# Performance work log

Measured on AMD Instinct MI355X. Metric: run time of the kernel, lower is better.

Reference implementation:

```python
import jax, jax.numpy as jnp
import numpy as np

HUGE = jnp.float32(1e31)  # ops.HUGE_INT


def setup_inputs() -> dict:
    key = jax.random.key(0)
    ks = jax.random.split(key, 11)
    B, A = 2048, 256
    NE, NR = 100000, 1000
    DE, DR, DH = 128, 128, 256
    act = DE + DR  # action_dim = W1 hidden width
    return {
        "e": jax.random.randint(ks[0], (B,), 0, NE),
        "q": jax.random.randint(ks[1], (B,), 0, NR),
        "H": jax.random.normal(ks[2], (B, DH), jnp.float32),
        "r_space": jax.random.randint(ks[3], (B, A), 0, NR),
        "r_mask": jnp.ones((B, A), jnp.float32),
        "entity_emb": jax.random.normal(ks[4], (NE, DE), jnp.float32),
        "rel_emb": jax.random.normal(ks[5], (NR, DR), jnp.float32),
        "W1": jax.random.normal(ks[6], (DE + DH + DR, act), jnp.float32) * 0.05,
        "b1": jnp.zeros((act,), jnp.float32),
        "W2": jax.random.normal(ks[7], (act, DR), jnp.float32) * 0.05,
        "b2": jnp.zeros((DR,), jnp.float32),
    }


def reference(e, q, H, r_space, r_mask, entity_emb, rel_emb, W1, b1, W2, b2):
    # Gather node / query embeddings (kg.get_entity_embeddings / get_relation_embeddings)
    E = entity_emb[e]              # [B, DE]
    Q = rel_emb[q]                 # [B, DR]
    X = jnp.concatenate([E, H, Q], axis=-1)        # [B, DE+DH+DR]
    X = jax.nn.relu(X @ W1 + b1)                   # W1 + ReLU
    X = X @ W2 + b2                                # W2 -> [B, DR]
    # Gather candidate relation embeddings for the (padded) action space
    R = rel_emb[r_space]                           # [B, A, DR]
    logit = jnp.einsum("bad,bd->ba", R, X)        # squeeze(R @ X.unsqueeze(2))
    logit = logit - (1.0 - r_mask) * HUGE          # mask invalid actions
    dist = jax.nn.softmax(logit, axis=-1)          # [B, A]
    entropy = -jnp.sum(dist * jnp.log(jnp.clip(dist, 1e-20, None)), axis=-1)  # ops.entropy
    return dist, entropy
```

## Files before the change

### kernel.cpp

```cpp
#include <hip/hip_runtime.h>


#define DE   128
#define DH   256
#define DR   128
#define DIN  512
#define ACT  256
#define AA   256
#define BB   8
#define NR   1000
#define SCL  1008

#define XS_P 520
#define HS_P 264
#define X2_P 136

#define W2B_OFF 16384
#define RB_OFF  20480
#define PREP_T  36608

typedef __attribute__((ext_vector_type(4))) float f32x4;
typedef __attribute__((ext_vector_type(8))) short s16x8;
typedef unsigned int u32;
typedef unsigned short u16;

#define MFMA(a,b,c) __builtin_amdgcn_mfma_f32_16x16x32_bf16(a, b, c, 0, 0, 0)

__device__ __forceinline__ u32 b16(float x) {
    u32 u = __float_as_uint(x);
    return (u + 0x7FFFu + ((u >> 16) & 1u)) >> 16;
}
__device__ __forceinline__ float b16f(u32 h) { return __uint_as_float(h << 16); }
__device__ __forceinline__ u32 pack2(float a, float b) { return b16(a) | (b16(b) << 16); }

__device__ __forceinline__ s16x8 asfrag(uint4 v) {
    union { uint4 u; s16x8 s; } c; c.u = v; return c.s;
}

__global__ __launch_bounds__(256) void prep_kernel(
    const float* __restrict__ W1, const float* __restrict__ W2,
    const float* __restrict__ rel_emb, uint4* __restrict__ wsb)
{
    const int id = blockIdx.x * 256 + threadIdx.x;
    const int l  = id & 63;
    const int tl = id >> 6;
    const int kb_l = (l >> 4) * 8;
    const int n_l  = l & 15;
    float f[8];
    if (tl < 256) {
        const int kt = tl >> 4, nt = tl & 15;
        const int kb = kt * 32 + kb_l, n = nt * 16 + n_l;
        #pragma unroll
        for (int i = 0; i < 8; ++i) f[i] = W1[(size_t)(kb + i) * ACT + n];
    } else if (tl < 320) {
        const int t2 = tl - 256;
        const int kt = t2 >> 3, nt = t2 & 7;
        const int kb = kt * 32 + kb_l, n = nt * 16 + n_l;
        #pragma unroll
        for (int i = 0; i < 8; ++i) f[i] = W2[(size_t)(kb + i) * DR + n];
    } else {
        const int t3 = tl - 320;
        const int nt = t3 >> 2, kt = t3 & 3;
        const int kb = kt * 32 + kb_l, n = nt * 16 + n_l;
        #pragma unroll
        for (int i = 0; i < 8; ++i)
            f[i] = (n < NR) ? rel_emb[(size_t)n * DR + kb + i] : 0.f;
    }
    uint4 o;
    o.x = pack2(f[0], f[1]); o.y = pack2(f[2], f[3]);
    o.z = pack2(f[4], f[5]); o.w = pack2(f[6], f[7]);
    wsb[id] = o;
}

__global__ __launch_bounds__(512, 2) void policy_kernel(
    const int*   __restrict__ e,
    const int*   __restrict__ q,
    const float* __restrict__ H,
    const int*   __restrict__ r_space,
    const float* __restrict__ r_mask,
    const float* __restrict__ entity_emb,
    const float* __restrict__ rel_emb,
    const float* __restrict__ b1,
    const float* __restrict__ b2,
    const uint4* __restrict__ wsb,
    float* __restrict__ dist_out,
    float* __restrict__ ent_out)
{
    const int t  = threadIdx.x;
    const int b0 = blockIdx.x * BB;
    const int l  = t & 63;
    const int w  = t >> 6;
    const int m  = l & 15;
    const int pl = m >> 3;
    const int rw = m & 7;
    const int kb_l = (l >> 4) * 8;

    __shared__ __align__(16) u16 xbf[2][BB][XS_P];
    __shared__ __align__(16) u16 hbf[2][BB][HS_P];
    __shared__ __align__(16) u16 x2bf[2][BB][X2_P];
    __shared__ float scoreL[BB * SCL];

    int   ridx[4];
    float msk [4];
    #pragma unroll
    for (int c = 0; c < 4; ++c) {
        ridx[c] = r_space[(size_t)(b0 + w) * AA + l + 64 * c];
        msk [c] = r_mask [(size_t)(b0 + w) * AA + l + 64 * c];
    }

    #pragma unroll
    for (int u = 0; u < 2; ++u) {
        const int j   = t + u * 512;
        const int row = j & 7;
        const int kq  = (j >> 3) * 4;
        const int sb  = b0 + row;
        float4 v;
        if (kq < DE)            v = *(const float4*)&entity_emb[(size_t)e[sb] * DE + kq];
        else if (kq < DE + DH)  v = *(const float4*)&H[(size_t)sb * DH + (kq - DE)];
        else                    v = *(const float4*)&rel_emb[(size_t)q[sb] * DR + (kq - DE - DH)];
        const float f[4] = {v.x, v.y, v.z, v.w};
        u32 hi[4], lo[4];
        #pragma unroll
        for (int i = 0; i < 4; ++i) {
            hi[i] = b16(f[i]);
            lo[i] = b16(f[i] - b16f(hi[i]));
        }
        uint2 ph, plv;
        ph.x  = hi[0] | (hi[1] << 16); ph.y  = hi[2] | (hi[3] << 16);
        plv.x = lo[0] | (lo[1] << 16); plv.y = lo[2] | (lo[3] << 16);
        *(uint2*)&xbf[0][row][kq] = ph;
        *(uint2*)&xbf[1][row][kq] = plv;
    }
    __syncthreads();

    {
        f32x4 acc0 = {0.f, 0.f, 0.f, 0.f};
        f32x4 acc1 = {0.f, 0.f, 0.f, 0.f};
        const int nt0 = 2 * w, nt1 = 2 * w + 1;
        const u16* abase = &xbf[pl][rw][kb_l];
        #pragma unroll
        for (int kt = 0; kt < 16; ++kt) {
            const uint4 af  = *(const uint4*)(abase + kt * 32);
            const uint4 bv0 = wsb[(size_t)(kt * 16 + nt0) * 64 + l];
            const uint4 bv1 = wsb[(size_t)(kt * 16 + nt1) * 64 + l];
            acc0 = MFMA(asfrag(af), asfrag(bv0), acc0);
            acc1 = MFMA(asfrag(af), asfrag(bv1), acc1);
        }
        #pragma unroll
        for (int v = 0; v < 4; ++v) {
            acc0[v] += __shfl_xor(acc0[v], 32, 64);
            acc1[v] += __shfl_xor(acc1[v], 32, 64);
        }
        if (l < 32) {
            const int r4 = (l >> 4) * 4;
            const int n0 = nt0 * 16 + m, n1 = nt1 * 16 + m;
            const float bb0 = b1[n0], bb1 = b1[n1];
            #pragma unroll
            for (int v = 0; v < 4; ++v) {
                const float h0 = fmaxf(acc0[v] + bb0, 0.f);
                const float h1 = fmaxf(acc1[v] + bb1, 0.f);
                const u32 h0h = b16(h0), h1h = b16(h1);
                hbf[0][r4 + v][n0] = (u16)h0h;
                hbf[1][r4 + v][n0] = (u16)b16(h0 - b16f(h0h));
                hbf[0][r4 + v][n1] = (u16)h1h;
                hbf[1][r4 + v][n1] = (u16)b16(h1 - b16f(h1h));
            }
        }
    }
    __syncthreads();

    {
        f32x4 acc = {0.f, 0.f, 0.f, 0.f};
        const u16* abase = &hbf[pl][rw][kb_l];
        #pragma unroll
        for (int kt = 0; kt < 8; ++kt) {
            const uint4 af = *(const uint4*)(abase + kt * 32);
            const uint4 bv = wsb[(size_t)(W2B_OFF + (kt * 8 + w) * 64 + l)];
            acc = MFMA(asfrag(af), asfrag(bv), acc);
        }
        #pragma unroll
        for (int v = 0; v < 4; ++v) acc[v] += __shfl_xor(acc[v], 32, 64);
        if (l < 32) {
            const int r4 = (l >> 4) * 4;
            const int n  = w * 16 + m;
            const float bb = b2[n];
            #pragma unroll
            for (int v = 0; v < 4; ++v) {
                const float x2 = acc[v] + bb;
                const u32 xh = b16(x2);
                x2bf[0][r4 + v][n] = (u16)xh;
                x2bf[1][r4 + v][n] = (u16)b16(x2 - b16f(xh));
            }
        }
    }
    __syncthreads();

    {
        uint4 sf[4];
        const u16* abase = &x2bf[pl][rw][kb_l];
        #pragma unroll
        for (int kt = 0; kt < 4; ++kt)
            sf[kt] = *(const uint4*)(abase + kt * 32);
        #pragma unroll 2
        for (int i = 0; i < 8; ++i) {
            const int nt = w * 8 + i;
            if (nt >= 63) break;
            f32x4 acc = {0.f, 0.f, 0.f, 0.f};
            #pragma unroll
            for (int kt = 0; kt < 4; ++kt) {
                const uint4 bv = wsb[(size_t)(RB_OFF + (nt * 4 + kt) * 64 + l)];
                acc = MFMA(asfrag(sf[kt]), asfrag(bv), acc);
            }
            #pragma unroll
            for (int v = 0; v < 4; ++v) acc[v] += __shfl_xor(acc[v], 32, 64);
            if (l < 32) {
                const int r4 = (l >> 4) * 4;
                const int n  = nt * 16 + m;
                #pragma unroll
                for (int v = 0; v < 4; ++v)
                    scoreL[(r4 + v) * SCL + n] = acc[v];
            }
        }
    }
    __syncthreads();

    {
        float lg[4];
        #pragma unroll
        for (int c = 0; c < 4; ++c)
            lg[c] = scoreL[w * SCL + ridx[c]] - (1.0f - msk[c]) * 1e31f;

        float mx = fmaxf(fmaxf(lg[0], lg[1]), fmaxf(lg[2], lg[3]));
        #pragma unroll
        for (int off = 32; off >= 1; off >>= 1)
            mx = fmaxf(mx, __shfl_xor(mx, off, 64));

        float p[4], S = 0.f, SLa = 0.f;
        #pragma unroll
        for (int c = 0; c < 4; ++c) {
            const float z = lg[c] - mx;
            p[c] = __expf(z);
            S   += p[c];
            SLa += p[c] * z;
        }
        #pragma unroll
        for (int off = 32; off >= 1; off >>= 1) {
            S   += __shfl_xor(S,   off, 64);
            SLa += __shfl_xor(SLa, off, 64);
        }

        const float inv = 1.0f / S;
        #pragma unroll
        for (int c = 0; c < 4; ++c)
            dist_out[(size_t)(b0 + w) * AA + l + 64 * c] = p[c] * inv;
        if (l == 0)
            ent_out[b0 + w] = __logf(S) - SLa * inv;
    }
}

extern "C" void kernel_launch(void* const* d_in, const int* in_sizes, int n_in,
                              void* d_out, int out_size, void* d_ws, size_t ws_size,
                              hipStream_t stream) {
    const int*   e          = (const int*)  d_in[0];
    const int*   q          = (const int*)  d_in[1];
    const float* H          = (const float*)d_in[2];
    const int*   r_space    = (const int*)  d_in[3];
    const float* r_mask     = (const float*)d_in[4];
    const float* entity_emb = (const float*)d_in[5];
    const float* rel_emb    = (const float*)d_in[6];
    const float* W1         = (const float*)d_in[7];
    const float* b1         = (const float*)d_in[8];
    const float* W2         = (const float*)d_in[9];
    const float* b2         = (const float*)d_in[10];

    const int B = in_sizes[0];
    float* dist_out = (float*)d_out;
    float* ent_out  = (float*)d_out + (size_t)B * AA;
    uint4* wsb      = (uint4*)d_ws;

    prep_kernel<<<PREP_T / 256, 256, 0, stream>>>(W1, W2, rel_emb, wsb);
    policy_kernel<<<B / BB, 512, 0, stream>>>(
        e, q, H, r_space, r_mask, entity_emb, rel_emb,
        b1, b2, wsb, dist_out, ent_out);
}
```

Baseline: 22.68 us.

## Double policy kernel block to 1024 threads, splitting layer-1 and score tiles across 16 waves

Launches the policy kernel with 1024 threads (16 waves) per block instead of 512. Each wave now computes one W1 output tile instead of two, and the relation-score GEMM spreads its 63 tiles over 16 waves, four each. The W2 layer and the softmax/entropy stage stay on the first 8 waves, so half the waves idle there. The aim is more parallelism and shorter per-wave MFMA chains. The cost is higher register pressure under launch_bounds(1024,2) and idle waves in the serial stages.

```diff
diff --git a/kernel.cpp b/kernel.cpp
--- a/kernel.cpp
+++ b/kernel.cpp
@@ -72,7 +72,7 @@
     wsb[id] = o;
 }
 
-__global__ __launch_bounds__(512, 2) void policy_kernel(
+__global__ __launch_bounds__(1024, 2) void policy_kernel(
     const int*   __restrict__ e,
     const int*   __restrict__ q,
     const float* __restrict__ H,
@@ -102,17 +102,17 @@
 
     int   ridx[4];
     float msk [4];
-    #pragma unroll
-    for (int c = 0; c < 4; ++c) {
-        ridx[c] = r_space[(size_t)(b0 + w) * AA + l + 64 * c];
-        msk [c] = r_mask [(size_t)(b0 + w) * AA + l + 64 * c];
-    }
-
-    #pragma unroll
-    for (int u = 0; u < 2; ++u) {
-        const int j   = t + u * 512;
-        const int row = j & 7;
-        const int kq  = (j >> 3) * 4;
+    if (w < 8) {
+        #pragma unroll
+        for (int c = 0; c < 4; ++c) {
+            ridx[c] = r_space[(size_t)(b0 + w) * AA + l + 64 * c];
+            msk [c] = r_mask [(size_t)(b0 + w) * AA + l + 64 * c];
+        }
+    }
+
+    {
+        const int row = t & 7;
+        const int kq  = (t >> 3) * 4;
         const int sb  = b0 + row;
         float4 v;
         if (kq < DE)            v = *(const float4*)&entity_emb[(size_t)e[sb] * DE + kq];
@@ -134,42 +134,33 @@
     __syncthreads();
 
     {
-        f32x4 acc0 = {0.f, 0.f, 0.f, 0.f};
-        f32x4 acc1 = {0.f, 0.f, 0.f, 0.f};
-        const int nt0 = 2 * w, nt1 = 2 * w + 1;
+        f32x4 acc = {0.f, 0.f, 0.f, 0.f};
         const u16* abase = &xbf[pl][rw][kb_l];
         #pragma unroll
         for (int kt = 0; kt < 16; ++kt) {
-            const uint4 af  = *(const uint4*)(abase + kt * 32);
-            const uint4 bv0 = wsb[(size_t)(kt * 16 + nt0) * 64 + l];
-            const uint4 bv1 = wsb[(size_t)(kt * 16 + nt1) * 64 + l];
-            acc0 = MFMA(asfrag(af), asfrag(bv0), acc0);
-            acc1 = MFMA(asfrag(af), asfrag(bv1), acc1);
-        }
-        #pragma unroll
-        for (int v = 0; v < 4; ++v) {
-            acc0[v] += __shfl_xor(acc0[v], 32, 64);
-            acc1[v] += __shfl_xor(acc1[v], 32, 64);
-        }
+            const uint4 af = *(const uint4*)(abase + kt * 32);
+            const uint4 bv = wsb[(size_t)(kt * 16 + w) * 64 + l];
+            acc = MFMA(asfrag(af), asfrag(bv), acc);
+        }
+        #pragma unroll
+        for (int v = 0; v < 4; ++v)
+            acc[v] += __shfl_xor(acc[v], 32, 64);
         if (l < 32) {
             const int r4 = (l >> 4) * 4;
-            const int n0 = nt0 * 16 + m, n1 = nt1 * 16 + m;
-            const float bb0 = b1[n0], bb1 = b1[n1];
+            const int n  = w * 16 + m;
+            const float bb = b1[n];
             #pragma unroll
             for (int v = 0; v < 4; ++v) {
-                const float h0 = fmaxf(acc0[v] + bb0, 0.f);
-                const float h1 = fmaxf(acc1[v] + bb1, 0.f);
-                const u32 h0h = b16(h0), h1h = b16(h1);
-                hbf[0][r4 + v][n0] = (u16)h0h;
-                hbf[1][r4 + v][n0] = (u16)b16(h0 - b16f(h0h));
-                hbf[0][r4 + v][n1] = (u16)h1h;
-                hbf[1][r4 + v][n1] = (u16)b16(h1 - b16f(h1h));
-            }
-        }
-    }
-    __syncthreads();
-
-    {
+                const float h = fmaxf(acc[v] + bb, 0.f);
+                const u32 hh = b16(h);
+                hbf[0][r4 + v][n] = (u16)hh;
+                hbf[1][r4 + v][n] = (u16)b16(h - b16f(hh));
+            }
+        }
+    }
+    __syncthreads();
+
+    if (w < 8) {
         f32x4 acc = {0.f, 0.f, 0.f, 0.f};
         const u16* abase = &hbf[pl][rw][kb_l];
         #pragma unroll
@@ -201,9 +192,9 @@
         #pragma unroll
         for (int kt = 0; kt < 4; ++kt)
             sf[kt] = *(const uint4*)(abase + kt * 32);
-        #pragma unroll 2
-        for (int i = 0; i < 8; ++i) {
-            const int nt = w * 8 + i;
+        #pragma unroll
+        for (int i = 0; i < 4; ++i) {
+            const int nt = w * 4 + i;
             if (nt >= 63) break;
             f32x4 acc = {0.f, 0.f, 0.f, 0.f};
             #pragma unroll
@@ -224,7 +215,7 @@
     }
     __syncthreads();
 
-    {
+    if (w < 8) {
         float lg[4];
         #pragma unroll
         for (int c = 0; c < 4; ++c)
@@ -279,7 +270,7 @@
     uint4* wsb      = (uint4*)d_ws;
 
     prep_kernel<<<PREP_T / 256, 256, 0, stream>>>(W1, W2, rel_emb, wsb);
-    policy_kernel<<<B / BB, 512, 0, stream>>>(
+    policy_kernel<<<B / BB, 1024, 0, stream>>>(
         e, q, H, r_space, r_mask, entity_emb, rel_emb,
         b1, b2, wsb, dist_out, ent_out);
 }
```

New measurement: 20.26 us, median of 3. 1.12x faster.
